# Optimization experiments

Hardware: AMD Instinct MI355X
Metric: run time of the kernel (lower is better)

The kernel has to match this reference:

```python
import jax, jax.numpy as jnp
import numpy as np

NUM_CAMS, BS, NUM_QUERY, MAX_LEN, EMBED_DIMS, NPTS = 6, 1, 40000, 10000, 256, 4


def setup_inputs() -> dict:
    key = jax.random.key(0)
    kq, kr, km = jax.random.split(key, 3)
    query = jax.random.normal(kq, (BS, NUM_QUERY, EMBED_DIMS), dtype=jnp.float32)
    reference_points_cam = jax.random.normal(
        kr, (NUM_CAMS, BS, NUM_QUERY, NPTS, 2), dtype=jnp.float32)
    bev_mask = jax.random.randint(km, (NUM_CAMS, BS, NUM_QUERY, NPTS), 0, 2).astype(jnp.int32)
    return {"query": query, "reference_points_cam": reference_points_cam, "bev_mask": bev_mask}


def reference(query, reference_points_cam, bev_mask):
    # valid[c, q]: query q is seen by camera c (any of the NPTS mask bits set); bs == 1
    valid = (bev_mask > 0).any(-1)            # (cams, bs, Q) bool
    valid0 = valid[:, 0]                      # (cams, Q)

    # Stable stream compaction: valid indices first, in ascending query order.
    order = jnp.argsort(~valid0, axis=-1, stable=True)      # (cams, Q)
    indexes = order[:, :MAX_LEN].astype(jnp.int32)          # (cams, max_len)
    indexes_len = jnp.minimum(valid0.sum(-1), MAX_LEN).astype(jnp.int32)  # (cams,)

    # Padded gather/rebatch; zero out slots beyond each camera's valid count.
    pos_ok = jnp.arange(MAX_LEN)[None, :] < indexes_len[:, None]          # (cams, max_len)
    queries_rebatch = query[0][indexes]                                   # (cams, max_len, E)
    queries_rebatch = jnp.where(pos_ok[:, :, None], queries_rebatch, 0.0)

    ref0 = reference_points_cam[:, 0]                                     # (cams, Q, NPTS, 2)
    reference_points_rebatch = jax.vmap(lambda r, i: r[i])(ref0, indexes) # (cams, max_len, NPTS, 2)
    reference_points_rebatch = jnp.where(
        pos_ok[:, :, None, None], reference_points_rebatch, 0.0)

    # count_norm: 1 / (number of cameras that see each query, clamped to >= 1)
    count = valid.astype(jnp.float32).sum(0)                 # (bs, Q)
    count_norm = (1.0 / jnp.maximum(count, 1.0))[..., None]  # (bs, Q, 1)

    return (indexes,
            indexes_len,
            queries_rebatch.reshape(BS * NUM_CAMS, MAX_LEN, EMBED_DIMS),
            reference_points_rebatch.reshape(BS * NUM_CAMS, MAX_LEN, NPTS, 2),
            count_norm)
```

## Files before the change

### kernel.cpp

```cpp
#include <hip/hip_runtime.h>
#include <hip/hip_bf16.h>

#define NUM_CAMS 6
#define NQ       40000
#define MAX_LEN  10000
#define ED       256
#define NBLK     ((NQ + 255) / 256)

typedef float f32x2 __attribute__((ext_vector_type(2)));

#define OFF_IDX  0
#define OFF_LEN  (NUM_CAMS * MAX_LEN)
#define OFF_Q    (OFF_LEN + NUM_CAMS)
#define OFF_REF  (OFF_Q + NUM_CAMS * MAX_LEN * ED)
#define OFF_CNT  (OFF_REF + NUM_CAMS * MAX_LEN * 8)

#define WS_OFF    0
#define WS_MASK_I 960
#define WS_MASK_N (NUM_CAMS * NBLK * 4)
#define WS_LEN    (WS_MASK_I + 2 * WS_MASK_N)
#define WS_POS    (WS_LEN + 8)
#define WS_NEED_BYTES ((WS_POS + NUM_CAMS * NQ) * 4)

#define QBLOCKS      (NQ / 4)
#define TAIL_BLOCKS  (NUM_CAMS * MAX_LEN / 4)
#define GATHER_GRID  2048
#define CNT_BLOCKS   ((NQ + 255) / 256)
#define GATHER_BLOCKS (NUM_CAMS * MAX_LEN / 4)

__global__ void kA_counts(const int* __restrict__ bev, float* __restrict__ out,
                          int* __restrict__ ws, int usePos) {
    __shared__ int cnt[NUM_CAMS];
    const int tid = threadIdx.x;
    const int blk = blockIdx.x;
    const int q   = blk * 256 + tid;
    if (tid < NUM_CAMS) cnt[tid] = 0;
    __syncthreads();
    const int lane = tid & 63;
    const int wave = tid >> 6;
    const bool inb = q < NQ;
    unsigned long long* wsm = reinterpret_cast<unsigned long long*>(ws + WS_MASK_I);
    int myCount = 0;
    #pragma unroll
    for (int cam = 0; cam < NUM_CAMS; ++cam) {
        bool v = false;
        if (inb) {
            const int4 m = *reinterpret_cast<const int4*>(bev + ((size_t)cam * NQ + q) * 4);
            v = (m.x > 0) | (m.y > 0) | (m.z > 0) | (m.w > 0);
        }
        myCount += v ? 1 : 0;
        const unsigned long long bal = __ballot(v);
        if (lane == 0) {
            atomicAdd(&cnt[cam], __popcll(bal));
            if (usePos) wsm[((size_t)cam * NBLK + blk) * 4 + wave] = bal;
        }
    }
    if (inb) out[OFF_CNT + q] = 1.0f / fmaxf((float)myCount, 1.0f);
    __syncthreads();
    if (tid < NUM_CAMS) ws[WS_OFF + tid * NBLK + blk] = cnt[tid];
}

__global__ void kBC_indexes(const int* __restrict__ bev, float* __restrict__ out,
                            int* __restrict__ ws, int usePos) {
    const int blk = blockIdx.x;
    const int cam = blockIdx.y;
    const int tid = threadIdx.x;
    const int lane = tid & 63;
    const int wave = tid >> 6;

    const int part = (tid < NBLK) ? ws[WS_OFF + cam * NBLK + tid] : 0;
    int t = part;
    int o = (tid < blk) ? part : 0;
    #pragma unroll
    for (int d = 1; d < 64; d <<= 1) {
        t += __shfl_xor(t, d, 64);
        o += __shfl_xor(o, d, 64);
    }
    __shared__ int sT[4], sO[4], waveSums[4];

    unsigned long long mask;
    if (usePos) {
        const unsigned long long* wsm =
            reinterpret_cast<const unsigned long long*>(ws + WS_MASK_I);
        mask = wsm[((size_t)cam * NBLK + blk) * 4 + wave];
    } else {
        const int q = blk * 256 + tid;
        bool v = false;
        if (q < NQ) {
            const int4 m = *reinterpret_cast<const int4*>(bev + ((size_t)cam * NQ + q) * 4);
            v = (m.x > 0) | (m.y > 0) | (m.z > 0) | (m.w > 0);
        }
        mask = __ballot(v);
    }
    if (lane == 0) { sT[wave] = t; sO[wave] = o; waveSums[wave] = __popcll(mask); }
    __syncthreads();
    const int total    = sT[0] + sT[1] + sT[2] + sT[3];
    const int blockOff = sO[0] + sO[1] + sO[2] + sO[3];

    if (blk == 0 && tid == 0) {
        const int len = total < MAX_LEN ? total : MAX_LEN;
        ws[WS_LEN + cam] = len;
        out[OFF_LEN + cam] = (float)len;
    }

    const int q = blk * 256 + tid;
    if (q < NQ) {
        int waveOff = 0;
        #pragma unroll
        for (int w = 0; w < 4; ++w)
            if (w < wave) waveOff += waveSums[w];
        const bool v     = (mask >> lane) & 1ull;
        const int prefix = __popcll(mask & ((1ull << lane) - 1ull));
        const int vb  = blockOff + waveOff + prefix;
        const int pos = v ? vb : (total + (q - vb));
        if (pos < MAX_LEN) out[OFF_IDX + cam * MAX_LEN + pos] = (float)q;
        if (usePos) ws[WS_POS + cam * NQ + q] = (v && vb < MAX_LEN) ? vb : -1;
    }
}

__global__ void kGatherQ(const float* __restrict__ query, const float* __restrict__ refp,
                         float* __restrict__ out, const int* __restrict__ ws) {
    const int tid   = threadIdx.x;
    const int group = tid >> 6;
    const int lane  = tid & 63;
    for (int item = blockIdx.x; item < QBLOCKS + TAIL_BLOCKS; item += gridDim.x) {
        if (item < QBLOCKS) {
            const int q = item * 4 + group;
            int pos[NUM_CAMS];
            bool any = false;
            #pragma unroll
            for (int cam = 0; cam < NUM_CAMS; ++cam) {
                const int p = ws[WS_POS + cam * NQ + q];
                pos[cam] = p;
                any |= (p >= 0);
            }
            if (!any) continue;

            const float4 vq = *reinterpret_cast<const float4*>(query + (size_t)q * ED + lane * 4);
            f32x2 a; a.x = vq.x; a.y = vq.y;
            f32x2 b; b.x = vq.z; b.y = vq.w;

            #pragma unroll
            for (int cam = 0; cam < NUM_CAMS; ++cam) {
                const int p = pos[cam];
                if (p >= 0) {
                    f32x2* o2 = reinterpret_cast<f32x2*>(out + OFF_Q + ((size_t)cam * MAX_LEN + p) * ED + lane * 4);
                    o2[0] = a;
                    o2[1] = b;
                    if (lane < 4) {
                        const f32x2 r = *reinterpret_cast<const f32x2*>(refp + ((size_t)cam * NQ + q) * 8 + lane * 2);
                        *reinterpret_cast<f32x2*>(out + OFF_REF + ((size_t)cam * MAX_LEN + p) * 8 + lane * 2) = r;
                    }
                }
            }
        } else {
            const int rowId = (item - QBLOCKS) * 4 + group;
            const int cam   = rowId / MAX_LEN;
            const int j     = rowId - cam * MAX_LEN;
            if (j < ws[WS_LEN + cam]) continue;
            const f32x2 z = (f32x2)(0.f);
            f32x2* o2 = reinterpret_cast<f32x2*>(out + OFF_Q + (size_t)rowId * ED + lane * 4);
            o2[0] = z; o2[1] = z;
            if (lane < 4)
                *reinterpret_cast<f32x2*>(out + OFF_REF + (size_t)rowId * 8 + lane * 2) = z;
        }
    }
}

__global__ void kGather(const float* __restrict__ query, const float* __restrict__ refp,
                        float* __restrict__ out, const int* __restrict__ ws,
                        const int* __restrict__ bev) {
    const int blk = blockIdx.x;
    const int tid = threadIdx.x;
    if (blk >= GATHER_BLOCKS) {
        const int q = (blk - GATHER_BLOCKS) * 256 + tid;
        if (q < NQ) {
            int cnt = 0;
            #pragma unroll
            for (int cam = 0; cam < NUM_CAMS; ++cam) {
                const int4 m = *reinterpret_cast<const int4*>(bev + ((size_t)cam * NQ + q) * 4);
                cnt += ((m.x > 0) | (m.y > 0) | (m.z > 0) | (m.w > 0)) ? 1 : 0;
            }
            out[OFF_CNT + q] = 1.0f / fmaxf((float)cnt, 1.0f);
        }
        return;
    }
    const int rowId = blk * 4 + (tid >> 6);
    const int lane  = tid & 63;
    const int cam   = rowId / MAX_LEN;
    const int j     = rowId - cam * MAX_LEN;
    const int len   = ws[WS_LEN + cam];

    f32x2 a = (f32x2)(0.f), b = (f32x2)(0.f), r0 = (f32x2)(0.f), r1 = (f32x2)(0.f);
    if (j < len) {
        const int idx = (int)out[OFF_IDX + cam * MAX_LEN + j];
        const float4 vq = *reinterpret_cast<const float4*>(query + (size_t)idx * ED + lane * 4);
        a.x = vq.x; a.y = vq.y;
        b.x = vq.z; b.y = vq.w;
        if (lane < 2) {
            const float4 r = *reinterpret_cast<const float4*>(refp + ((size_t)cam * NQ + idx) * 8 + lane * 4);
            r0.x = r.x; r0.y = r.y;
            r1.x = r.z; r1.y = r.w;
        }
    }
    f32x2* o2 = reinterpret_cast<f32x2*>(out + OFF_Q + (size_t)rowId * ED + lane * 4);
    o2[0] = a;
    o2[1] = b;
    if (lane < 2) {
        f32x2* r2 = reinterpret_cast<f32x2*>(out + OFF_REF + (size_t)rowId * 8 + lane * 4);
        r2[0] = r0;
        r2[1] = r1;
    }
}

extern "C" void kernel_launch(void* const* d_in, const int* in_sizes, int n_in,
                              void* d_out, int out_size, void* d_ws, size_t ws_size,
                              hipStream_t stream) {
    const float* query = (const float*)d_in[0];
    const float* refp  = (const float*)d_in[1];
    const int*   bev   = (const int*)d_in[2];
    float* out = (float*)d_out;
    int*   ws  = (int*)d_ws;
    const int usePos = (ws_size >= (size_t)WS_NEED_BYTES) ? 1 : 0;

    kA_counts<<<NBLK, 256, 0, stream>>>(bev, out, ws, usePos);
    kBC_indexes<<<dim3(NBLK, NUM_CAMS), 256, 0, stream>>>(bev, out, ws, usePos);
    if (usePos) {
        kGatherQ<<<GATHER_GRID, 256, 0, stream>>>(query, refp, out, ws);
    } else {
        kGather<<<GATHER_BLOCKS + CNT_BLOCKS, 256, 0, stream>>>(query, refp, out, ws, bev);
    }
}
```

Baseline: 30.99 us.

## Fuse index compaction into gather kernel, recomputing positions from ballot masks

Removes the separate index kernel and its per-query position array. Each block of the fused kernel recomputes the per-camera block prefix sums in shared memory and derives each query's compacted position from the stored wave ballot masks. It then writes the index output and scatters query and reference rows. This saves one launch and the position-array round trip, but every block redundantly scans the 157 block counts per camera. Index writes also become single-lane per query instead of coalesced.

```diff
diff --git a/kernel.cpp b/kernel.cpp
--- a/kernel.cpp
+++ b/kernel.cpp
@@ -8,6 +8,7 @@
 #define NBLK     ((NQ + 255) / 256)
 
 typedef float f32x2 __attribute__((ext_vector_type(2)));
+typedef unsigned long long u64;
 
 #define OFF_IDX  0
 #define OFF_LEN  (NUM_CAMS * MAX_LEN)
@@ -15,21 +16,20 @@
 #define OFF_REF  (OFF_Q + NUM_CAMS * MAX_LEN * ED)
 #define OFF_CNT  (OFF_REF + NUM_CAMS * MAX_LEN * 8)
 
-#define WS_OFF    0
+#define WS_CNT    0
 #define WS_MASK_I 960
-#define WS_MASK_N (NUM_CAMS * NBLK * 4)
-#define WS_LEN    (WS_MASK_I + 2 * WS_MASK_N)
-#define WS_POS    (WS_LEN + 8)
-#define WS_NEED_BYTES ((WS_POS + NUM_CAMS * NQ) * 4)
+#define WS_MASK_INTS (NUM_CAMS * NBLK * 4 * 2)
+#define WS_NEED_BYTES ((WS_MASK_I + WS_MASK_INTS) * 4)
+#define FB_LEN    (WS_MASK_I + WS_MASK_INTS)
 
 #define QBLOCKS      (NQ / 4)
 #define TAIL_BLOCKS  (NUM_CAMS * MAX_LEN / 4)
-#define GATHER_GRID  2048
-#define CNT_BLOCKS   ((NQ + 255) / 256)
+#define ALL_GRID     2048
 #define GATHER_BLOCKS (NUM_CAMS * MAX_LEN / 4)
-
-__global__ void kA_counts(const int* __restrict__ bev, float* __restrict__ out,
-                          int* __restrict__ ws, int usePos) {
+#define CNT_BLOCKS   NBLK
+
+__global__ void kMeta(const int* __restrict__ bev, float* __restrict__ out,
+                      int* __restrict__ ws) {
     __shared__ int cnt[NUM_CAMS];
     const int tid = threadIdx.x;
     const int blk = blockIdx.x;
@@ -39,7 +39,7 @@
     const int lane = tid & 63;
     const int wave = tid >> 6;
     const bool inb = q < NQ;
-    unsigned long long* wsm = reinterpret_cast<unsigned long long*>(ws + WS_MASK_I);
+    u64* wsm = reinterpret_cast<u64*>(ws + WS_MASK_I);
     int myCount = 0;
     #pragma unroll
     for (int cam = 0; cam < NUM_CAMS; ++cam) {
@@ -49,26 +49,123 @@
             v = (m.x > 0) | (m.y > 0) | (m.z > 0) | (m.w > 0);
         }
         myCount += v ? 1 : 0;
-        const unsigned long long bal = __ballot(v);
+        const u64 bal = __ballot(v);
         if (lane == 0) {
             atomicAdd(&cnt[cam], __popcll(bal));
-            if (usePos) wsm[((size_t)cam * NBLK + blk) * 4 + wave] = bal;
+            wsm[((size_t)cam * NBLK + blk) * 4 + wave] = bal;
         }
     }
     if (inb) out[OFF_CNT + q] = 1.0f / fmaxf((float)myCount, 1.0f);
     __syncthreads();
-    if (tid < NUM_CAMS) ws[WS_OFF + tid * NBLK + blk] = cnt[tid];
-}
-
-__global__ void kBC_indexes(const int* __restrict__ bev, float* __restrict__ out,
-                            int* __restrict__ ws, int usePos) {
+    if (tid < NUM_CAMS) ws[WS_CNT + tid * NBLK + blk] = cnt[tid];
+}
+
+__global__ __launch_bounds__(256) void kAll(const float* __restrict__ query,
+                                            const float* __restrict__ refp,
+                                            float* __restrict__ out,
+                                            const int* __restrict__ ws) {
+    __shared__ int sOff[NUM_CAMS][NBLK + 3];
+    __shared__ int sTot[NUM_CAMS], sLen[NUM_CAMS];
+    const int tid  = threadIdx.x;
+    const int lane = tid & 63;
+    const int wave = tid >> 6;
+
+    for (int cam = wave; cam < NUM_CAMS; cam += 4) {
+        int running = 0;
+        for (int base = 0; base < NBLK; base += 64) {
+            const int i = base + lane;
+            const int val = (i < NBLK) ? ws[WS_CNT + cam * NBLK + i] : 0;
+            int v = val;
+            #pragma unroll
+            for (int d = 1; d < 64; d <<= 1) {
+                const int n = __shfl_up(v, d, 64);
+                if (lane >= d) v += n;
+            }
+            if (i < NBLK) sOff[cam][i] = running + v - val;
+            running += __shfl(v, 63, 64);
+        }
+        if (lane == 0) {
+            sTot[cam] = running;
+            sLen[cam] = running < MAX_LEN ? running : MAX_LEN;
+        }
+    }
+    __syncthreads();
+    if (blockIdx.x == 0 && tid < NUM_CAMS) out[OFF_LEN + tid] = (float)sLen[tid];
+
+    const u64* __restrict__ wsm = reinterpret_cast<const u64*>(ws + WS_MASK_I);
+
+    for (int item = blockIdx.x; item < QBLOCKS + TAIL_BLOCKS; item += gridDim.x) {
+        if (item < QBLOCKS) {
+            const int q  = item * 4 + wave;
+            const int qb = q >> 8;
+            const int qw = (q >> 6) & 3;
+            const int ql = q & 63;
+            int pos[NUM_CAMS];
+            bool any = false;
+            #pragma unroll
+            for (int c = 0; c < NUM_CAMS; ++c) {
+                const u64* mp = wsm + ((size_t)c * NBLK + qb) * 4;
+                const u64 m0 = mp[0], m1 = mp[1], m2 = mp[2], m3 = mp[3];
+                const u64 mq = qw == 0 ? m0 : qw == 1 ? m1 : qw == 2 ? m2 : m3;
+                int pre = 0;
+                if (qw > 0) pre += __popcll(m0);
+                if (qw > 1) pre += __popcll(m1);
+                if (qw > 2) pre += __popcll(m2);
+                const bool v  = (mq >> ql) & 1ull;
+                const int  vb = sOff[c][qb] + pre + __popcll(mq & ((1ull << ql) - 1ull));
+                pos[c] = (v && vb < MAX_LEN) ? vb : -1;
+                any |= pos[c] >= 0;
+                if (lane == 0) {
+                    if (v) {
+                        if (vb < MAX_LEN) out[OFF_IDX + c * MAX_LEN + vb] = (float)q;
+                    } else {
+                        const int pi = sTot[c] + (q - vb);
+                        if (pi < MAX_LEN) out[OFF_IDX + c * MAX_LEN + pi] = (float)q;
+                    }
+                }
+            }
+            if (!any) continue;
+
+            const float4 vq = *reinterpret_cast<const float4*>(query + (size_t)q * ED + lane * 4);
+            f32x2 a; a.x = vq.x; a.y = vq.y;
+            f32x2 b; b.x = vq.z; b.y = vq.w;
+
+            #pragma unroll
+            for (int c = 0; c < NUM_CAMS; ++c) {
+                const int p = pos[c];
+                if (p >= 0) {
+                    f32x2* o2 = reinterpret_cast<f32x2*>(out + OFF_Q + ((size_t)c * MAX_LEN + p) * ED + lane * 4);
+                    o2[0] = a;
+                    o2[1] = b;
+                    if (lane < 4) {
+                        const f32x2 r = *reinterpret_cast<const f32x2*>(refp + ((size_t)c * NQ + q) * 8 + lane * 2);
+                        *reinterpret_cast<f32x2*>(out + OFF_REF + ((size_t)c * MAX_LEN + p) * 8 + lane * 2) = r;
+                    }
+                }
+            }
+        } else {
+            const int rowId = (item - QBLOCKS) * 4 + wave;
+            const int c = rowId / MAX_LEN;
+            const int j = rowId - c * MAX_LEN;
+            if (j < sLen[c]) continue;
+            const f32x2 z = (f32x2)(0.f);
+            f32x2* o2 = reinterpret_cast<f32x2*>(out + OFF_Q + (size_t)rowId * ED + lane * 4);
+            o2[0] = z; o2[1] = z;
+            if (lane < 4)
+                *reinterpret_cast<f32x2*>(out + OFF_REF + (size_t)rowId * 8 + lane * 2) = z;
+        }
+    }
+}
+
+__global__ void kBC_fb(const int* __restrict__ bev, float* __restrict__ out,
+                       int* __restrict__ ws) {
     const int blk = blockIdx.x;
     const int cam = blockIdx.y;
     const int tid = threadIdx.x;
     const int lane = tid & 63;
     const int wave = tid >> 6;
 
-    const int part = (tid < NBLK) ? ws[WS_OFF + cam * NBLK + tid] : 0;
+    const int part = (tid < NBLK) ? ws[WS_CNT + cam * NBLK + tid] : 0;
     int t = part;
     int o = (tid < blk) ? part : 0;
     #pragma unroll
@@ -78,20 +175,13 @@
     }
     __shared__ int sT[4], sO[4], waveSums[4];
 
-    unsigned long long mask;
-    if (usePos) {
-        const unsigned long long* wsm =
-            reinterpret_cast<const unsigned long long*>(ws + WS_MASK_I);
-        mask = wsm[((size_t)cam * NBLK + blk) * 4 + wave];
-    } else {
-        const int q = blk * 256 + tid;
-        bool v = false;
-        if (q < NQ) {
-            const int4 m = *reinterpret_cast<const int4*>(bev + ((size_t)cam * NQ + q) * 4);
-            v = (m.x > 0) | (m.y > 0) | (m.z > 0) | (m.w > 0);
-        }
-        mask = __ballot(v);
-    }
+    const int q = blk * 256 + tid;
+    bool v = false;
+    if (q < NQ) {
+        const int4 m = *reinterpret_cast<const int4*>(bev + ((size_t)cam * NQ + q) * 4);
+        v = (m.x > 0) | (m.y > 0) | (m.z > 0) | (m.w > 0);
+    }
+    const u64 mask = __ballot(v);
     if (lane == 0) { sT[wave] = t; sO[wave] = o; waveSums[wave] = __popcll(mask); }
     __syncthreads();
     const int total    = sT[0] + sT[1] + sT[2] + sT[3];
@@ -99,97 +189,28 @@
 
     if (blk == 0 && tid == 0) {
         const int len = total < MAX_LEN ? total : MAX_LEN;
-        ws[WS_LEN + cam] = len;
+        ws[FB_LEN + cam] = len;
         out[OFF_LEN + cam] = (float)len;
     }
-
-    const int q = blk * 256 + tid;
     if (q < NQ) {
         int waveOff = 0;
         #pragma unroll
         for (int w = 0; w < 4; ++w)
             if (w < wave) waveOff += waveSums[w];
-        const bool v     = (mask >> lane) & 1ull;
         const int prefix = __popcll(mask & ((1ull << lane) - 1ull));
         const int vb  = blockOff + waveOff + prefix;
         const int pos = v ? vb : (total + (q - vb));
         if (pos < MAX_LEN) out[OFF_IDX + cam * MAX_LEN + pos] = (float)q;
-        if (usePos) ws[WS_POS + cam * NQ + q] = (v && vb < MAX_LEN) ? vb : -1;
-    }
-}
-
-__global__ void kGatherQ(const float* __restrict__ query, const float* __restrict__ refp,
-                         float* __restrict__ out, const int* __restrict__ ws) {
-    const int tid   = threadIdx.x;
-    const int group = tid >> 6;
-    const int lane  = tid & 63;
-    for (int item = blockIdx.x; item < QBLOCKS + TAIL_BLOCKS; item += gridDim.x) {
-        if (item < QBLOCKS) {
-            const int q = item * 4 + group;
-            int pos[NUM_CAMS];
-            bool any = false;
-            #pragma unroll
-            for (int cam = 0; cam < NUM_CAMS; ++cam) {
-                const int p = ws[WS_POS + cam * NQ + q];
-                pos[cam] = p;
-                any |= (p >= 0);
-            }
-            if (!any) continue;
-
-            const float4 vq = *reinterpret_cast<const float4*>(query + (size_t)q * ED + lane * 4);
-            f32x2 a; a.x = vq.x; a.y = vq.y;
-            f32x2 b; b.x = vq.z; b.y = vq.w;
-
-            #pragma unroll
-            for (int cam = 0; cam < NUM_CAMS; ++cam) {
-                const int p = pos[cam];
-                if (p >= 0) {
-                    f32x2* o2 = reinterpret_cast<f32x2*>(out + OFF_Q + ((size_t)cam * MAX_LEN + p) * ED + lane * 4);
-                    o2[0] = a;
-                    o2[1] = b;
-                    if (lane < 4) {
-                        const f32x2 r = *reinterpret_cast<const f32x2*>(refp + ((size_t)cam * NQ + q) * 8 + lane * 2);
-                        *reinterpret_cast<f32x2*>(out + OFF_REF + ((size_t)cam * MAX_LEN + p) * 8 + lane * 2) = r;
-                    }
-                }
-            }
-        } else {
-            const int rowId = (item - QBLOCKS) * 4 + group;
-            const int cam   = rowId / MAX_LEN;
-            const int j     = rowId - cam * MAX_LEN;
-            if (j < ws[WS_LEN + cam]) continue;
-            const f32x2 z = (f32x2)(0.f);
-            f32x2* o2 = reinterpret_cast<f32x2*>(out + OFF_Q + (size_t)rowId * ED + lane * 4);
-            o2[0] = z; o2[1] = z;
-            if (lane < 4)
-                *reinterpret_cast<f32x2*>(out + OFF_REF + (size_t)rowId * 8 + lane * 2) = z;
-        }
-    }
-}
-
-__global__ void kGather(const float* __restrict__ query, const float* __restrict__ refp,
-                        float* __restrict__ out, const int* __restrict__ ws,
-                        const int* __restrict__ bev) {
-    const int blk = blockIdx.x;
-    const int tid = threadIdx.x;
-    if (blk >= GATHER_BLOCKS) {
-        const int q = (blk - GATHER_BLOCKS) * 256 + tid;
-        if (q < NQ) {
-            int cnt = 0;
-            #pragma unroll
-            for (int cam = 0; cam < NUM_CAMS; ++cam) {
-                const int4 m = *reinterpret_cast<const int4*>(bev + ((size_t)cam * NQ + q) * 4);
-                cnt += ((m.x > 0) | (m.y > 0) | (m.z > 0) | (m.w > 0)) ? 1 : 0;
-            }
-            out[OFF_CNT + q] = 1.0f / fmaxf((float)cnt, 1.0f);
-        }
-        return;
-    }
-    const int rowId = blk * 4 + (tid >> 6);
-    const int lane  = tid & 63;
+    }
+}
+
+__global__ void kGather_fb(const float* __restrict__ query, const float* __restrict__ refp,
+                           float* __restrict__ out, const int* __restrict__ ws) {
+    const int rowId = blockIdx.x * 4 + (threadIdx.x >> 6);
+    const int lane  = threadIdx.x & 63;
     const int cam   = rowId / MAX_LEN;
     const int j     = rowId - cam * MAX_LEN;
-    const int len   = ws[WS_LEN + cam];
+    const int len   = ws[FB_LEN + cam];
 
     f32x2 a = (f32x2)(0.f), b = (f32x2)(0.f), r0 = (f32x2)(0.f), r1 = (f32x2)(0.f);
     if (j < len) {
@@ -221,13 +242,12 @@
     const int*   bev   = (const int*)d_in[2];
     float* out = (float*)d_out;
     int*   ws  = (int*)d_ws;
-    const int usePos = (ws_size >= (size_t)WS_NEED_BYTES) ? 1 : 0;
-
-    kA_counts<<<NBLK, 256, 0, stream>>>(bev, out, ws, usePos);
-    kBC_indexes<<<dim3(NBLK, NUM_CAMS), 256, 0, stream>>>(bev, out, ws, usePos);
-    if (usePos) {
-        kGatherQ<<<GATHER_GRID, 256, 0, stream>>>(query, refp, out, ws);
+
+    kMeta<<<NBLK, 256, 0, stream>>>(bev, out, ws);
+    if (ws_size >= (size_t)WS_NEED_BYTES + 64) {
+        kAll<<<ALL_GRID, 256, 0, stream>>>(query, refp, out, ws);
     } else {
-        kGather<<<GATHER_BLOCKS + CNT_BLOCKS, 256, 0, stream>>>(query, refp, out, ws, bev);
-    }
-}
+        kBC_fb<<<dim3(NBLK, NUM_CAMS), 256, 0, stream>>>(bev, out, ws);
+        kGather_fb<<<GATHER_BLOCKS, 256, 0, stream>>>(query, refp, out, ws);
+    }
+}
```

New measurement: 46.01 us. 1.48x slower.

## Replace query-major scatter gather with row-major indexed gather kernel

Applied to the files above, without the earlier changes.

Drops the per-query scatter kernel, which read a position table of cams by NQ and scattered each query row to up to six cameras with a separate zero-fill pass. It now always runs a row-major gather: one wave per output row reads the compacted index and loads the query and reference row, writing zeros beyond len. This removes the position-table writes and reads from the index kernel and gives fully coalesced contiguous output writes. The cost is a dependent index load per row and random query reads instead of streaming ones.

```diff
diff --git a/kernel.cpp b/kernel.cpp
--- a/kernel.cpp
+++ b/kernel.cpp
@@ -8,6 +8,7 @@
 #define NBLK     ((NQ + 255) / 256)
 
 typedef float f32x2 __attribute__((ext_vector_type(2)));
+typedef unsigned long long u64;
 
 #define OFF_IDX  0
 #define OFF_LEN  (NUM_CAMS * MAX_LEN)
@@ -19,17 +20,12 @@
 #define WS_MASK_I 960
 #define WS_MASK_N (NUM_CAMS * NBLK * 4)
 #define WS_LEN    (WS_MASK_I + 2 * WS_MASK_N)
-#define WS_POS    (WS_LEN + 8)
-#define WS_NEED_BYTES ((WS_POS + NUM_CAMS * NQ) * 4)
+#define WS_NEED_BYTES ((WS_LEN + 8) * 4)
 
-#define QBLOCKS      (NQ / 4)
-#define TAIL_BLOCKS  (NUM_CAMS * MAX_LEN / 4)
-#define GATHER_GRID  2048
-#define CNT_BLOCKS   ((NQ + 255) / 256)
 #define GATHER_BLOCKS (NUM_CAMS * MAX_LEN / 4)
 
 __global__ void kA_counts(const int* __restrict__ bev, float* __restrict__ out,
-                          int* __restrict__ ws, int usePos) {
+                          int* __restrict__ ws, int useMask) {
     __shared__ int cnt[NUM_CAMS];
     const int tid = threadIdx.x;
     const int blk = blockIdx.x;
@@ -39,7 +35,7 @@
     const int lane = tid & 63;
     const int wave = tid >> 6;
     const bool inb = q < NQ;
-    unsigned long long* wsm = reinterpret_cast<unsigned long long*>(ws + WS_MASK_I);
+    u64* wsm = reinterpret_cast<u64*>(ws + WS_MASK_I);
     int myCount = 0;
     #pragma unroll
     for (int cam = 0; cam < NUM_CAMS; ++cam) {
@@ -49,10 +45,10 @@
             v = (m.x > 0) | (m.y > 0) | (m.z > 0) | (m.w > 0);
         }
         myCount += v ? 1 : 0;
-        const unsigned long long bal = __ballot(v);
+        const u64 bal = __ballot(v);
         if (lane == 0) {
             atomicAdd(&cnt[cam], __popcll(bal));
-            if (usePos) wsm[((size_t)cam * NBLK + blk) * 4 + wave] = bal;
+            if (useMask) wsm[((size_t)cam * NBLK + blk) * 4 + wave] = bal;
         }
     }
     if (inb) out[OFF_CNT + q] = 1.0f / fmaxf((float)myCount, 1.0f);
@@ -61,7 +57,7 @@
 }
 
 __global__ void kBC_indexes(const int* __restrict__ bev, float* __restrict__ out,
-                            int* __restrict__ ws, int usePos) {
+                            int* __restrict__ ws, int useMask) {
     const int blk = blockIdx.x;
     const int cam = blockIdx.y;
     const int tid = threadIdx.x;
@@ -78,10 +74,9 @@
     }
     __shared__ int sT[4], sO[4], waveSums[4];
 
-    unsigned long long mask;
-    if (usePos) {
-        const unsigned long long* wsm =
-            reinterpret_cast<const unsigned long long*>(ws + WS_MASK_I);
+    u64 mask;
+    if (useMask) {
+        const u64* wsm = reinterpret_cast<const u64*>(ws + WS_MASK_I);
         mask = wsm[((size_t)cam * NBLK + blk) * 4 + wave];
     } else {
         const int q = blk * 256 + tid;
@@ -114,79 +109,13 @@
         const int vb  = blockOff + waveOff + prefix;
         const int pos = v ? vb : (total + (q - vb));
         if (pos < MAX_LEN) out[OFF_IDX + cam * MAX_LEN + pos] = (float)q;
-        if (usePos) ws[WS_POS + cam * NQ + q] = (v && vb < MAX_LEN) ? vb : -1;
     }
 }
 
-__global__ void kGatherQ(const float* __restrict__ query, const float* __restrict__ refp,
-                         float* __restrict__ out, const int* __restrict__ ws) {
-    const int tid   = threadIdx.x;
-    const int group = tid >> 6;
-    const int lane  = tid & 63;
-    for (int item = blockIdx.x; item < QBLOCKS + TAIL_BLOCKS; item += gridDim.x) {
-        if (item < QBLOCKS) {
-            const int q = item * 4 + group;
-            int pos[NUM_CAMS];
-            bool any = false;
-            #pragma unroll
-            for (int cam = 0; cam < NUM_CAMS; ++cam) {
-                const int p = ws[WS_POS + cam * NQ + q];
-                pos[cam] = p;
-                any |= (p >= 0);
-            }
-            if (!any) continue;
-
-            const float4 vq = *reinterpret_cast<const float4*>(query + (size_t)q * ED + lane * 4);
-            f32x2 a; a.x = vq.x; a.y = vq.y;
-            f32x2 b; b.x = vq.z; b.y = vq.w;
-
-            #pragma unroll
-            for (int cam = 0; cam < NUM_CAMS; ++cam) {
-                const int p = pos[cam];
-                if (p >= 0) {
-                    f32x2* o2 = reinterpret_cast<f32x2*>(out + OFF_Q + ((size_t)cam * MAX_LEN + p) * ED + lane * 4);
-                    o2[0] = a;
-                    o2[1] = b;
-                    if (lane < 4) {
-                        const f32x2 r = *reinterpret_cast<const f32x2*>(refp + ((size_t)cam * NQ + q) * 8 + lane * 2);
-                        *reinterpret_cast<f32x2*>(out + OFF_REF + ((size_t)cam * MAX_LEN + p) * 8 + lane * 2) = r;
-                    }
-                }
-            }
-        } else {
-            const int rowId = (item - QBLOCKS) * 4 + group;
-            const int cam   = rowId / MAX_LEN;
-            const int j     = rowId - cam * MAX_LEN;
-            if (j < ws[WS_LEN + cam]) continue;
-            const f32x2 z = (f32x2)(0.f);
-            f32x2* o2 = reinterpret_cast<f32x2*>(out + OFF_Q + (size_t)rowId * ED + lane * 4);
-            o2[0] = z; o2[1] = z;
-            if (lane < 4)
-                *reinterpret_cast<f32x2*>(out + OFF_REF + (size_t)rowId * 8 + lane * 2) = z;
-        }
-    }
-}
-
-__global__ void kGather(const float* __restrict__ query, const float* __restrict__ refp,
-                        float* __restrict__ out, const int* __restrict__ ws,
-                        const int* __restrict__ bev) {
-    const int blk = blockIdx.x;
-    const int tid = threadIdx.x;
-    if (blk >= GATHER_BLOCKS) {
-        const int q = (blk - GATHER_BLOCKS) * 256 + tid;
-        if (q < NQ) {
-            int cnt = 0;
-            #pragma unroll
-            for (int cam = 0; cam < NUM_CAMS; ++cam) {
-                const int4 m = *reinterpret_cast<const int4*>(bev + ((size_t)cam * NQ + q) * 4);
-                cnt += ((m.x > 0) | (m.y > 0) | (m.z > 0) | (m.w > 0)) ? 1 : 0;
-            }
-            out[OFF_CNT + q] = 1.0f / fmaxf((float)cnt, 1.0f);
-        }
-        return;
-    }
-    const int rowId = blk * 4 + (tid >> 6);
-    const int lane  = tid & 63;
+__global__ void kGatherRM(const float* __restrict__ query, const float* __restrict__ refp,
+                          float* __restrict__ out, const int* __restrict__ ws) {
+    const int rowId = blockIdx.x * 4 + (threadIdx.x >> 6);
+    const int lane  = threadIdx.x & 63;
     const int cam   = rowId / MAX_LEN;
     const int j     = rowId - cam * MAX_LEN;
     const int len   = ws[WS_LEN + cam];
@@ -221,13 +150,9 @@
     const int*   bev   = (const int*)d_in[2];
     float* out = (float*)d_out;
     int*   ws  = (int*)d_ws;
-    const int usePos = (ws_size >= (size_t)WS_NEED_BYTES) ? 1 : 0;
+    const int useMask = (ws_size >= (size_t)WS_NEED_BYTES) ? 1 : 0;
 
-    kA_counts<<<NBLK, 256, 0, stream>>>(bev, out, ws, usePos);
-    kBC_indexes<<<dim3(NBLK, NUM_CAMS), 256, 0, stream>>>(bev, out, ws, usePos);
-    if (usePos) {
-        kGatherQ<<<GATHER_GRID, 256, 0, stream>>>(query, refp, out, ws);
-    } else {
-        kGather<<<GATHER_BLOCKS + CNT_BLOCKS, 256, 0, stream>>>(query, refp, out, ws, bev);
-    }
+    kA_counts<<<NBLK, 256, 0, stream>>>(bev, out, ws, useMask);
+    kBC_indexes<<<dim3(NBLK, NUM_CAMS), 256, 0, stream>>>(bev, out, ws, useMask);
+    kGatherRM<<<GATHER_BLOCKS, 256, 0, stream>>>(query, refp, out, ws);
 }
```

New measurement: 32.53 us. +5.0%, slower.
